# Kernel tuning notes

Measured on AMD Instinct MI355X. Metric: run time of the kernel, lower is better.

The kernel has to match this reference:

```python
import jax, jax.numpy as jnp
import numpy as np

B, DIM, W0, H0 = 4, 256, 128, 128
HEADS, HEAD_DIM = 8, 32
FOLD, PROP = 2, 4
EPS_GN = 1e-5


def _l2norm(x):
    n = jnp.linalg.norm(x, axis=-1, keepdims=True)
    return x / jnp.maximum(n, 1e-12)  # matches F.normalize eps


def _fold(t, f):
    # (b, c, f*w, f*h) -> (b*f*f, c, w, h), matching einops '(b f1 f2)' ordering
    b, c, W, H = t.shape
    w, h = W // f, H // f
    return t.reshape(b, c, f, w, f, h).transpose(0, 2, 4, 1, 3, 5).reshape(b * f * f, c, w, h)


def _unfold(t, f, b0):
    bf, c, w, h = t.shape
    return t.reshape(b0, f, f, c, w, h).transpose(0, 3, 1, 4, 2, 5).reshape(b0, c, f * w, f * h)


def _pool(t, p):
    # AdaptiveAvgPool2d((p, p)) for divisible sizes
    b, c, w, h = t.shape
    return t.reshape(b, c, p, w // p, p, h // p).mean(axis=(3, 5))


def setup_inputs() -> dict:
    key = jax.random.key(0)
    ks = jax.random.split(key, 6)
    D = HEADS * HEAD_DIM
    return {
        "x": jax.random.normal(ks[0], (B, DIM, W0, H0), jnp.float32),
        "xyz": jax.random.normal(ks[1], (B, 3, W0, H0), jnp.float32),
        "Wv": jax.random.normal(ks[2], (D, DIM, 7, 7), jnp.float32) * 0.02,
        "bv": jnp.zeros((D,), jnp.float32),
        "Wproj": jax.random.normal(ks[3], (DIM, D), jnp.float32) * 0.02,
        "bproj": jnp.zeros((DIM,), jnp.float32),
        "gn_w": jnp.ones((D,), jnp.float32),
        "gn_b": jnp.zeros((D,), jnp.float32),
        "sim_alpha": jnp.ones((1,), jnp.float32),
        "sim_beta": jnp.zeros((1,), jnp.float32),
    }


def reference(x, xyz, Wv, bv, Wproj, bproj, gn_w, gn_b, sim_alpha, sim_beta):
    # value = self.v(x): 7x7 conv, padding 3
    value = jax.lax.conv_general_dilated(
        x, Wv, (1, 1), ((3, 3), (3, 3)),
        dimension_numbers=("NCHW", "OIHW", "NCHW")) + bv[None, :, None, None]
    b0 = x.shape[0]
    # heads split: 'b (e c) w h -> (b e) c w h'
    xh = x.reshape(b0 * HEADS, HEAD_DIM, W0, H0)
    vh = value.reshape(b0 * HEADS, HEAD_DIM, W0, H0)
    xf = _fold(xh, FOLD)
    vf = _fold(vh, FOLD)
    xyzf = _fold(xyz, FOLD)
    bb, c, w, h = xf.shape
    M = PROP * PROP
    N = w * h
    centers = _pool(xf, PROP)                                   # (bb, c, p, p)
    xyz_c = _pool(xyzf, PROP)
    value_centers = _pool(vf, PROP).reshape(bb, c, M).transpose(0, 2, 1)  # (bb, M, c)
    cen = centers.reshape(bb, c, M).transpose(0, 2, 1)          # (bb, M, c)
    xpts = xf.reshape(bb, c, N).transpose(0, 2, 1)              # (bb, N, c)
    vpts = vf.reshape(bb, c, N).transpose(0, 2, 1)              # (bb, N, c)
    sim = jax.nn.sigmoid(sim_beta + sim_alpha *
                         jnp.einsum('bmc,bnc->bmn', _l2norm(cen), _l2norm(xpts)))
    bg = xyzf.shape[0]
    xyz_pts = xyzf.reshape(bg, 3, N).transpose(0, 2, 1)
    xyz_cc = xyz_c.reshape(bg, 3, M).transpose(0, 2, 1)
    sim_geo = jax.nn.sigmoid(sim_beta + sim_alpha *
                             jnp.einsum('bmc,bnc->bmn', _l2norm(xyz_cc), _l2norm(xyz_pts)))
    sim_geo = jnp.tile(sim_geo, (sim.shape[0] // sim_geo.shape[0], 1, 1))  # torch .repeat
    sim = sim * sim_geo ** 2
    # faithful mask math: scatter_(1, argmax, 1.0) into an all-ones tensor leaves it all-ones,
    # so dense_mask == 1 and split_mask == 0 exactly as in the source.
    dense_mask = jnp.ones_like(sim)
    split_mask = 1.0 - dense_mask
    denss_sim = sim * dense_mask
    split_sim = sim * split_mask
    split_out = (jnp.einsum('bmn,bnc->bmc', split_sim, vpts) + value_centers) \
                / (split_sim.sum(-1, keepdims=True) + 1.0)
    denss_out = (jnp.einsum('bmn,bnc->bmc', denss_sim, xpts) + cen) \
                / (denss_sim.sum(-1, keepdims=True) + 1.0)
    denss_pts = jnp.einsum('bmc,bmn->bnc', denss_out, denss_sim)  # (bb, N, c)
    split_pts = jnp.einsum('bmc,bmn->bnc', split_out, split_sim)
    out = (denss_pts + split_pts).transpose(0, 2, 1).reshape(bb, c, w, h)
    out = _unfold(out, FOLD, b0 * HEADS)
    out = out.reshape(b0, HEADS * HEAD_DIM, W0, H0)
    # GroupNorm with 1 group: normalize over (C, H, W) per sample
    mu = out.mean(axis=(1, 2, 3), keepdims=True)
    var = ((out - mu) ** 2).mean(axis=(1, 2, 3), keepdims=True)
    out = (out - mu) / jnp.sqrt(var + EPS_GN)
    out = out * gn_w[None, :, None, None] + gn_b[None, :, None, None]
    # proj 1x1 conv + silu
    out = jnp.einsum('bchw,oc->bohw', out, Wproj) + bproj[None, :, None, None]
    return jax.nn.silu(out)
```

## Files before the change

kernel.cpp:

```cpp
#include <hip/hip_runtime.h>
#include <stdint.h>


typedef __attribute__((ext_vector_type(8))) short short8;
typedef __attribute__((ext_vector_type(4))) float floatx4;
typedef __fp16 fp16x2 __attribute__((ext_vector_type(2)));

#define SIMW 264

__device__ float g_sbp[256];
__device__ float g_bias[1024];
__device__ __attribute__((aligned(16))) _Float16 g_Wa[4*256*256];
__device__ float g_cenraw[128*16*32];
__device__ float g_cenhat[128*16*32];
__device__ float g_gcenhat[16*16*4];
__device__ __attribute__((aligned(16))) _Float16 g_sim[(size_t)128*4096*16];
__device__ float g_dnum[128*16*16*32];
__device__ float g_Gp[(size_t)128*16*256];
__device__ float g_rsum[128*16*16];
__device__ __attribute__((aligned(16))) unsigned g_dnh2[128*256];

static __device__ __forceinline__ fp16x2 as_h2(unsigned u) { return __builtin_bit_cast(fp16x2, u); }
static __device__ __forceinline__ unsigned pk(float a, float b) {
  return __builtin_bit_cast(unsigned, __builtin_amdgcn_cvt_pkrtz(a, b));
}
static __device__ __forceinline__ float h16(float v) {
  return (float)as_h2(pk(v, 0.f))[0];
}
#if __has_builtin(__builtin_amdgcn_fdot2)
static __device__ __forceinline__ float fdot2(fp16x2 a, fp16x2 b, float c) {
  return __builtin_amdgcn_fdot2(a, b, c, false);
}
#else
static __device__ __forceinline__ float fdot2(fp16x2 a, fp16x2 b, float c) {
  return c + (float)a[0]*(float)b[0] + (float)a[1]*(float)b[1];
}
#endif
static __device__ __forceinline__ float sum16(const float* p) {
  const float4* q = (const float4*)p;
  float4 a = q[0], b = q[1], c = q[2], d = q[3];
  return (a.x+a.y+a.z+a.w) + (b.x+b.y+b.z+b.w) + (c.x+c.y+c.z+c.w) + (d.x+d.y+d.z+d.w);
}
static __device__ __forceinline__ float sigm(float z) {
  return __builtin_amdgcn_rcpf(1.f + __expf(-z));
}

__global__ __launch_bounds__(64) void k0_geo(const float* __restrict__ xyz) {
  __shared__ float gc[64];
  const int gti = blockIdx.x;
  const int bg = gti >> 2, f1 = (gti >> 1) & 1, f2 = gti & 1;
  const int t = threadIdx.x;
  if (t < 48) {
    const int m = t / 3, ch = t - 3*(t/3);
    const int pi = m >> 2, pj = m & 3;
    const float* p = xyz + (size_t)(bg*3+ch)*16384 + (f1*64 + pi*16)*128 + f2*64 + pj*16;
    float s = 0.f;
    #pragma unroll
    for (int r = 0; r < 16; ++r) s += sum16(p + r*128);
    gc[m*4+ch] = s * (1.f/256.f);
  }
  __syncthreads();
  if (t < 16) {
    float g0 = gc[t*4], g1 = gc[t*4+1], g2 = gc[t*4+2];
    float inv = 1.f / fmaxf(sqrtf(g0*g0+g1*g1+g2*g2), 1e-12f);
    float* o = g_gcenhat + gti*64 + t*4;
    o[0] = g0*inv; o[1] = g1*inv; o[2] = g2*inv; o[3] = 0.f;
  }
}

__global__ __launch_bounds__(128) void k1a_cen(const float* __restrict__ x) {
  __shared__ float cenL[128];
  __shared__ float invL[4];
  const int blk = blockIdx.x;
  const int bb = blk >> 2, pi = blk & 3;
  const int b = bb >> 5, e = (bb >> 2) & 7, f1 = (bb >> 1) & 1, f2 = bb & 1;
  const int tid = threadIdx.x;
  const int c = tid >> 2, pj = tid & 3;
  const int m = pi*4 + pj;
  const float* p = x + ((size_t)(b*256 + e*32 + c)*128 + f1*64 + pi*16)*128 + f2*64 + pj*16;
  float s = 0.f;
  #pragma unroll
  for (int r = 0; r < 16; ++r) s += sum16(p + r*128);
  const float raw = s * (1.f/256.f);
  cenL[pj*32 + c] = raw;
  g_cenraw[(bb*16 + m)*32 + c] = raw;
  __syncthreads();
  if (tid < 4) {
    float ss = 0.f;
    #pragma unroll
    for (int cc = 0; cc < 32; ++cc) { float v = cenL[tid*32+cc]; ss += v*v; }
    invL[tid] = 1.f / fmaxf(sqrtf(ss), 1e-12f);
  }
  __syncthreads();
  g_cenhat[(bb*16 + m)*32 + c] = raw * invL[pj];
}

__global__ __launch_bounds__(256, 4) void k1b_sim(const float* __restrict__ x,
                                                  const float* __restrict__ xyz,
                                                  const float* __restrict__ salpha,
                                                  const float* __restrict__ sbeta) {
  __shared__ __attribute__((aligned(16))) unsigned  xL[256*20];
  __shared__ __attribute__((aligned(16))) _Float16 simS[16*SIMW];
  __shared__ __attribute__((aligned(16))) _Float16 gT[16*SIMW];
  __shared__ __attribute__((aligned(16))) unsigned chP[16*16];
  __shared__ float gcenL[64];
  __shared__ float rsW[4*16];
  __shared__ float dnumL[512];
  float* GL = (float*)gT;
  const int blk = blockIdx.x;
  const int bb = blk >> 4, ck = blk & 15;
  const int b = bb >> 5, e = (bb >> 2) & 7, f1 = (bb >> 1) & 1, f2 = bb & 1;
  const int gti = ((e & 3) << 2) | (f1 << 1) | f2;
  const int tid = threadIdx.x, lane = tid & 63, wave = tid >> 6;
  const int lm = lane & 15, quad = lane >> 4;
  const float alpha = salpha[0], beta = sbeta[0];
  const float* xt = x + (((size_t)(b*256 + e*32))*128 + f1*64)*128 + f2*64;

  {
    const float2 cp = *(const float2*)(g_cenhat + bb*512 + tid*2);
    chP[tid] = pk(cp.x, cp.y);
  }
  if (tid < 64) gcenL[tid] = g_gcenhat[gti*64 + tid];
  dnumL[tid] = 0.f; dnumL[tid + 256] = 0.f;
  __syncthreads();

  const int ng = ck*256 + tid;
  const int wi = ng >> 6, hi = ng & 63;
  const int addr = wi*128 + hi;
  {
    float ss = 0.f;
    unsigned xp[16];
    #pragma unroll
    for (int p = 0; p < 16; ++p) {
      const float v0 = xt[(size_t)(2*p)*16384 + addr];
      const float v1 = xt[(size_t)(2*p+1)*16384 + addr];
      ss += v0*v0 + v1*v1;
      xp[p] = pk(v0, v1);
    }
    uint4 u0 = {xp[0],xp[1],xp[2],xp[3]};
    uint4 u1 = {xp[4],xp[5],xp[6],xp[7]};
    uint4 u2 = {xp[8],xp[9],xp[10],xp[11]};
    uint4 u3 = {xp[12],xp[13],xp[14],xp[15]};
    *(uint4*)(xL + tid*20)      = u0;
    *(uint4*)(xL + tid*20 + 4)  = u1;
    *(uint4*)(xL + tid*20 + 8)  = u2;
    *(uint4*)(xL + tid*20 + 12) = u3;
    const float invn = __builtin_amdgcn_rcpf(fmaxf(sqrtf(ss), 1e-12f));
    ((float*)xL)[tid*20 + 16] = invn;
  }
  {
    const float* gp = xyz + (size_t)((e & 3)*3)*16384 + (f1*64 + wi)*128 + f2*64 + hi;
    float g0 = gp[0], g1 = gp[16384], g2 = gp[32768];
    const float invg = __builtin_amdgcn_rcpf(fmaxf(sqrtf(g0*g0+g1*g1+g2*g2), 1e-12f));
    g0 *= invg; g1 *= invg; g2 *= invg;
    #pragma unroll
    for (int m = 0; m < 16; ++m) {
      const float* gh = gcenL + m*4;
      const float dg = gh[0]*g0 + gh[1]*g1 + gh[2]*g2;
      const float gg = sigm(beta + alpha*dg);
      gT[m*SIMW + tid] = (_Float16)(gg*gg);
    }
  }
  __syncthreads();

  {
    const short8 afx = *(const short8*)((const _Float16*)chP + lm*32 + quad*8);
    float rsacc[4] = {0.f, 0.f, 0.f, 0.f};
    #pragma unroll
    for (int t = 0; t < 4; ++t) {
      const int px = wave*64 + t*16 + lm;
      const short8 bfx = *(const short8*)((const _Float16*)xL + px*40 + quad*8);
      floatx4 d = {0.f,0.f,0.f,0.f};
      d = __builtin_amdgcn_mfma_f32_16x16x32_f16(afx, bfx, d, 0, 0, 0);
      const float invn = ((const float*)xL)[px*20 + 16];
      #pragma unroll
      for (int r = 0; r < 4; ++r) {
        const int m = quad*4 + r;
        const float gg2 = (float)gT[m*SIMW + px];
        const float sv = sigm(beta + alpha * d[r] * invn) * gg2;
        rsacc[r] += sv;
        simS[m*SIMW + px] = (_Float16)sv;
      }
    }
    #pragma unroll
    for (int r = 0; r < 4; ++r) {
      float v = rsacc[r];
      v += __shfl_xor(v, 1, 64); v += __shfl_xor(v, 2, 64);
      v += __shfl_xor(v, 4, 64); v += __shfl_xor(v, 8, 64);
      if (lm == 0) rsW[wave*16 + quad*4 + r] = v;
    }
  }
  __syncthreads();
  if (tid < 256) GL[tid] = 0.f;
  __syncthreads();

  {
    unsigned w[8];
    const unsigned short* sp = (const unsigned short*)simS;
    #pragma unroll
    for (int p = 0; p < 8; ++p)
      w[p] = (unsigned)sp[(2*p)*SIMW + tid] | ((unsigned)sp[(2*p+1)*SIMW + tid] << 16);
    _Float16* gp = g_sim + ((size_t)bb*4096 + ng)*16;
    *(uint4*)gp       = *(const uint4*)&w[0];
    *(uint4*)(gp + 8) = *(const uint4*)&w[4];
  }
  if (tid < 16)
    g_rsum[(bb*16 + ck)*16 + tid] = rsW[tid] + rsW[16+tid] + rsW[32+tid] + rsW[48+tid];

  {
    floatx4 acc0 = {0.f,0.f,0.f,0.f}, acc1 = {0.f,0.f,0.f,0.f};
    floatx4 accG = {0.f,0.f,0.f,0.f};
    #pragma unroll
    for (int ks = 0; ks < 2; ++ks) {
      const int kb = wave*64 + ks*32 + quad*8;
      const short8 af = *(const short8*)(simS + lm*SIMW + kb);
      const int ag = ck*512 + ((kb >> 6)*128) + (kb & 63);
      const float* pb0 = xt + (size_t)lm*16384 + ag;
      const float* pb1 = pb0 + (size_t)16*16384;
      short8 bf0, bf1;
      #pragma unroll
      for (int t = 0; t < 8; ++t) bf0[t] = __builtin_bit_cast(short, (_Float16)pb0[t]);
      #pragma unroll
      for (int t = 0; t < 8; ++t) bf1[t] = __builtin_bit_cast(short, (_Float16)pb1[t]);
      acc0 = __builtin_amdgcn_mfma_f32_16x16x32_f16(af, bf0, acc0, 0, 0, 0);
      acc1 = __builtin_amdgcn_mfma_f32_16x16x32_f16(af, bf1, acc1, 0, 0, 0);
      accG = __builtin_amdgcn_mfma_f32_16x16x32_f16(af, af,  accG, 0, 0, 0);
    }
    #pragma unroll
    for (int r = 0; r < 4; ++r) {
      atomicAdd(&dnumL[(quad*4 + r)*32 + lm],      acc0[r]);
      atomicAdd(&dnumL[(quad*4 + r)*32 + 16 + lm], acc1[r]);
      atomicAdd(&GL[(quad*4 + r)*16 + lm],         accG[r]);
    }
  }
  __syncthreads();
  g_dnum[(size_t)(bb*16 + ck)*512 + tid]       = dnumL[tid];
  g_dnum[(size_t)(bb*16 + ck)*512 + 256 + tid] = dnumL[tid + 256];
  g_Gp[(size_t)(bb*16 + ck)*256 + tid]         = GL[tid];
}

__global__ __launch_bounds__(512) void k1c_red() {
  __shared__ float denssL[512];
  __shared__ float rsL[16];
  __shared__ float red[16];
  const int bb = blockIdx.x, tid = threadIdx.x, lane = tid & 63, wv = tid >> 6;
  if (tid < 16) {
    float r = 1.f;
    #pragma unroll
    for (int k = 0; k < 16; ++k) r += g_rsum[(bb*16 + k)*16 + tid];
    rsL[tid] = r;
  }
  float a = g_cenraw[bb*512 + tid];
  #pragma unroll
  for (int k = 0; k < 16; ++k) a += g_dnum[(size_t)bb*8192 + k*512 + tid];
  __syncthreads();
  denssL[tid] = a / rsL[tid >> 5];
  __syncthreads();
  if (tid < 256) {
    const int c = tid >> 3, mp = tid & 7;
    g_dnh2[bb*256 + c*8 + mp] = pk(denssL[(2*mp)*32 + c], denssL[(2*mp+1)*32 + c]);
  }
  float contrib = 0.f;
  if (tid < 256) {
    const int m = tid >> 4, m2 = tid & 15;
    float g = 0.f;
    #pragma unroll
    for (int k = 0; k < 16; ++k) g += g_Gp[((size_t)bb*16 + k)*256 + tid];
    float p = 0.f;
    #pragma unroll
    for (int c = 0; c < 32; ++c)
      p += h16(denssL[m*32 + c]) * h16(denssL[m2*32 + c]);
    contrib = g * p;
  }
  float s1t = 0.f;
  if (tid < 16) {
    float sc = 0.f;
    #pragma unroll
    for (int c = 0; c < 32; ++c) sc += h16(denssL[tid*32 + c]);
    s1t = (rsL[tid] - 1.f) * sc;
  }
  #pragma unroll
  for (int off = 1; off < 64; off <<= 1) {
    contrib += __shfl_xor(contrib, off, 64);
    s1t     += __shfl_xor(s1t, off, 64);
  }
  if (lane == 0) { red[wv] = contrib; red[8 + wv] = s1t; }
  __syncthreads();
  if (tid == 0) {
    float s2 = 0.f, s1 = 0.f;
    #pragma unroll
    for (int w = 0; w < 8; ++w) { s2 += red[w]; s1 += red[8 + w]; }
    g_sbp[bb*2]     = s1;
    g_sbp[bb*2 + 1] = s2;
  }
}

__global__ __launch_bounds__(256) void k2_prep(const float* __restrict__ Wp,
                                               const float* __restrict__ bpr,
                                               const float* __restrict__ gnw,
                                               const float* __restrict__ gnb) {
  __shared__ float betaL[256];
  __shared__ float alphaL[256];
  __shared__ float S12[2];
  const int b = blockIdx.x, t = threadIdx.x;
  if (t < 64) {
    float v1 = 0.f, v2 = 0.f;
    if (t < 32) { v1 = g_sbp[(b*32 + t)*2]; v2 = g_sbp[(b*32 + t)*2 + 1]; }
    #pragma unroll
    for (int off = 1; off < 64; off <<= 1) { v1 += __shfl_xor(v1, off, 64); v2 += __shfl_xor(v2, off, 64); }
    if (t == 0) { S12[0] = v1; S12[1] = v2; }
  }
  __syncthreads();
  const float S1 = S12[0];
  const float S2 = S12[1];
  const float inv_n = 1.f / 4194304.f;
  const float mu  = S1 * inv_n;
  const float inv = rsqrtf(fmaxf(S2*inv_n - mu*mu, 0.f) + 1e-5f);
  const float a = inv * gnw[t];
  alphaL[t] = a;
  betaL[t] = gnb[t] - mu * a;
  __syncthreads();
  float k = bpr[t];
  const float* wr = Wp + t*256;
  _Float16* wa = g_Wa + ((size_t)b*256 + t)*256;
  for (int c = 0; c < 256; c += 8) {
    const float4 w0 = *(const float4*)(wr + c);
    const float4 w1 = *(const float4*)(wr + c + 4);
    k += w0.x*betaL[c+0] + w0.y*betaL[c+1] + w0.z*betaL[c+2] + w0.w*betaL[c+3]
       + w1.x*betaL[c+4] + w1.y*betaL[c+5] + w1.z*betaL[c+6] + w1.w*betaL[c+7];
    uint4 o;
    o.x = pk(w0.x*alphaL[c+0], w0.y*alphaL[c+1]);
    o.y = pk(w0.z*alphaL[c+2], w0.w*alphaL[c+3]);
    o.z = pk(w1.x*alphaL[c+4], w1.y*alphaL[c+5]);
    o.w = pk(w1.z*alphaL[c+6], w1.w*alphaL[c+7]);
    *(uint4*)(wa + c) = o;
  }
  g_bias[b*256 + t] = k;
}

__global__ __launch_bounds__(256, 4) void kf_proj(float* __restrict__ out) {
  __shared__ __attribute__((aligned(16))) _Float16 preL[64*256];
  __shared__ float biasL[256];
  const int blk = blockIdx.x;
  const int b = blk >> 8, pb = blk & 255;
  const int f1 = pb >> 7, f2 = pb & 1;
  const int nbase = ((pb >> 1) & 63) * 64;
  const int tid = threadIdx.x, lane = tid & 63, wave = tid >> 6;
  const int lm = lane & 15, quad = lane >> 4;
  const int m0 = wave*64;
  biasL[tid] = g_bias[b*256 + tid];

  #pragma unroll
  for (int eh = 0; eh < 2; ++eh) {
    const int e = wave*2 + eh;
    const int bb = b*32 + e*4 + f1*2 + f2;
    short8 bf0 = {}, bf1 = {};
    if (quad < 2) {
      const _Float16* dp = (const _Float16*)g_dnh2 + (size_t)bb*512 + quad*8;
      bf0 = *(const short8*)(dp + lm*16);
      bf1 = *(const short8*)(dp + (16 + lm)*16);
    }
    #pragma unroll
    for (int pt = 0; pt < 4; ++pt) {
      const short8 af = *(const short8*)(g_sim
          + ((size_t)bb*4096 + nbase + pt*16 + lm)*16 + (quad & 1)*8);
      floatx4 c0 = {0.f,0.f,0.f,0.f}, c1 = {0.f,0.f,0.f,0.f};
      c0 = __builtin_amdgcn_mfma_f32_16x16x32_f16(af, bf0, c0, 0, 0, 0);
      c1 = __builtin_amdgcn_mfma_f32_16x16x32_f16(af, bf1, c1, 0, 0, 0);
      #pragma unroll
      for (int r = 0; r < 4; ++r) {
        const int px = pt*16 + quad*4 + r;
        const int swz = (px & 7) << 4;
        const int b0 = (px*512 + (e*32 + lm)*2) ^ swz;
        const int b1 = (px*512 + (e*32 + 16 + lm)*2) ^ swz;
        *(_Float16*)((char*)preL + b0) = (_Float16)c0[r];
        *(_Float16*)((char*)preL + b1) = (_Float16)c1[r];
      }
    }
  }
  __syncthreads();

  floatx4 acc[4][4] = {};
  #pragma unroll
  for (int ks = 0; ks < 8; ++ks) {
    const _Float16* abase = g_Wa + ((size_t)b*256)*256 + (size_t)ks*32 + quad*8;
    short8 afr[4], bfr[4];
    #pragma unroll
    for (int mi = 0; mi < 4; ++mi)
      afr[mi] = *(const short8*)(abase + (size_t)(m0 + mi*16 + lm)*256);
    #pragma unroll
    for (int ni = 0; ni < 4; ++ni) {
      const int row = ni*16 + lm;
      const int byte = (row*512 + ks*64 + quad*16) ^ ((row & 7) << 4);
      bfr[ni] = *(const short8*)((const char*)preL + byte);
    }
    #pragma unroll
    for (int mi = 0; mi < 4; ++mi) {
      #pragma unroll
      for (int ni = 0; ni < 4; ++ni)
        acc[mi][ni] = __builtin_amdgcn_mfma_f32_16x16x32_f16(afr[mi], bfr[ni], acc[mi][ni], 0, 0, 0);
    }
  }
  #pragma unroll
  for (int mi = 0; mi < 4; ++mi) {
    #pragma unroll
    for (int r = 0; r < 4; ++r) {
      const int o = m0 + mi*16 + quad*4 + r;
      const float kb = biasL[o];
      #pragma unroll
      for (int ni = 0; ni < 4; ++ni) {
        float val = acc[mi][ni][r] + kb;
        val = val * sigm(val);
        out[((size_t)(b*256 + o))*16384 + pb*64 + ni*16 + lm] = val;
      }
    }
  }
}

extern "C" void kernel_launch(void* const* d_in, const int* in_sizes, int n_in,
                              void* d_out, int out_size, void* d_ws, size_t ws_size,
                              hipStream_t stream)
{
  (void)in_sizes; (void)n_in; (void)d_ws; (void)ws_size; (void)out_size;
  const float* x     = (const float*)d_in[0];
  const float* xyz   = (const float*)d_in[1];
  const float* Wproj = (const float*)d_in[4];
  const float* bproj = (const float*)d_in[5];
  const float* gnw   = (const float*)d_in[6];
  const float* gnb   = (const float*)d_in[7];
  const float* sa    = (const float*)d_in[8];
  const float* sb    = (const float*)d_in[9];
  float* out = (float*)d_out;

  hipLaunchKernelGGL(k0_geo,  dim3(16),   dim3(64),  0, stream, xyz);
  hipLaunchKernelGGL(k1a_cen, dim3(512),  dim3(128), 0, stream, x);
  hipLaunchKernelGGL(k1b_sim, dim3(2048), dim3(256), 0, stream, x, xyz, sa, sb);
  hipLaunchKernelGGL(k1c_red, dim3(128),  dim3(512), 0, stream);
  hipLaunchKernelGGL(k2_prep, dim3(4),    dim3(256), 0, stream, Wproj, bproj, gnw, gnb);
  hipLaunchKernelGGL(kf_proj, dim3(1024), dim3(256), 0, stream, out);
}
```

Before: 260.1 us.

## Merge pooling kernels, drop gT buffer and LDS atomics in sim kernel

Merges the xyz-pooling and x-pooling kernels into one launch with block-range dispatch. In the similarity kernel, the per-pixel geometric gate is no longer precomputed into a shared fp16 table; it is recomputed inline from normalized xyz stored next to the inverse norm. The LDS atomicAdd reduction of the MFMA partials is replaced by per-wave stores into an overlay of the xL buffer followed by a plain 4-way sum. Together these cut shared-memory use enough to raise launch bounds to 5 blocks per CU. The trade-off is some redundant sigmoid work per quad and reuse of xL after a barrier.

```diff
diff --git a/kernel.cpp b/kernel.cpp
--- a/kernel.cpp
+++ b/kernel.cpp
@@ -45,68 +45,66 @@
   return __builtin_amdgcn_rcpf(1.f + __expf(-z));
 }
 
-__global__ __launch_bounds__(64) void k0_geo(const float* __restrict__ xyz) {
-  __shared__ float gc[64];
-  const int gti = blockIdx.x;
-  const int bg = gti >> 2, f1 = (gti >> 1) & 1, f2 = gti & 1;
-  const int t = threadIdx.x;
-  if (t < 48) {
-    const int m = t / 3, ch = t - 3*(t/3);
-    const int pi = m >> 2, pj = m & 3;
-    const float* p = xyz + (size_t)(bg*3+ch)*16384 + (f1*64 + pi*16)*128 + f2*64 + pj*16;
-    float s = 0.f;
-    #pragma unroll
-    for (int r = 0; r < 16; ++r) s += sum16(p + r*128);
-    gc[m*4+ch] = s * (1.f/256.f);
-  }
-  __syncthreads();
-  if (t < 16) {
-    float g0 = gc[t*4], g1 = gc[t*4+1], g2 = gc[t*4+2];
-    float inv = 1.f / fmaxf(sqrtf(g0*g0+g1*g1+g2*g2), 1e-12f);
-    float* o = g_gcenhat + gti*64 + t*4;
-    o[0] = g0*inv; o[1] = g1*inv; o[2] = g2*inv; o[3] = 0.f;
-  }
-}
-
-__global__ __launch_bounds__(128) void k1a_cen(const float* __restrict__ x) {
+__global__ __launch_bounds__(128) void k01_pool(const float* __restrict__ x,
+                                                const float* __restrict__ xyz) {
   __shared__ float cenL[128];
   __shared__ float invL[4];
+  __shared__ float gc[64];
   const int blk = blockIdx.x;
-  const int bb = blk >> 2, pi = blk & 3;
-  const int b = bb >> 5, e = (bb >> 2) & 7, f1 = (bb >> 1) & 1, f2 = bb & 1;
   const int tid = threadIdx.x;
-  const int c = tid >> 2, pj = tid & 3;
-  const int m = pi*4 + pj;
-  const float* p = x + ((size_t)(b*256 + e*32 + c)*128 + f1*64 + pi*16)*128 + f2*64 + pj*16;
-  float s = 0.f;
-  #pragma unroll
-  for (int r = 0; r < 16; ++r) s += sum16(p + r*128);
-  const float raw = s * (1.f/256.f);
-  cenL[pj*32 + c] = raw;
-  g_cenraw[(bb*16 + m)*32 + c] = raw;
-  __syncthreads();
-  if (tid < 4) {
-    float ss = 0.f;
-    #pragma unroll
-    for (int cc = 0; cc < 32; ++cc) { float v = cenL[tid*32+cc]; ss += v*v; }
-    invL[tid] = 1.f / fmaxf(sqrtf(ss), 1e-12f);
-  }
-  __syncthreads();
-  g_cenhat[(bb*16 + m)*32 + c] = raw * invL[pj];
-}
-
-__global__ __launch_bounds__(256, 4) void k1b_sim(const float* __restrict__ x,
+  if (blk < 512) {
+    const int bb = blk >> 2, pi = blk & 3;
+    const int b = bb >> 5, e = (bb >> 2) & 7, f1 = (bb >> 1) & 1, f2 = bb & 1;
+    const int c = tid >> 2, pj = tid & 3;
+    const int m = pi*4 + pj;
+    const float* p = x + ((size_t)(b*256 + e*32 + c)*128 + f1*64 + pi*16)*128 + f2*64 + pj*16;
+    float s = 0.f;
+    #pragma unroll
+    for (int r = 0; r < 16; ++r) s += sum16(p + r*128);
+    const float raw = s * (1.f/256.f);
+    cenL[pj*32 + c] = raw;
+    g_cenraw[(bb*16 + m)*32 + c] = raw;
+    __syncthreads();
+    if (tid < 4) {
+      float ss = 0.f;
+      #pragma unroll
+      for (int cc = 0; cc < 32; ++cc) { float v = cenL[tid*32+cc]; ss += v*v; }
+      invL[tid] = 1.f / fmaxf(sqrtf(ss), 1e-12f);
+    }
+    __syncthreads();
+    g_cenhat[(bb*16 + m)*32 + c] = raw * invL[pj];
+  } else {
+    const int gti = blk - 512;
+    const int bg = gti >> 2, f1 = (gti >> 1) & 1, f2 = gti & 1;
+    if (tid < 48) {
+      const int m = tid / 3, ch = tid - 3*(tid/3);
+      const int pi = m >> 2, pj = m & 3;
+      const float* p = xyz + (size_t)(bg*3+ch)*16384 + (f1*64 + pi*16)*128 + f2*64 + pj*16;
+      float s = 0.f;
+      #pragma unroll
+      for (int r = 0; r < 16; ++r) s += sum16(p + r*128);
+      gc[m*4+ch] = s * (1.f/256.f);
+    }
+    __syncthreads();
+    if (tid < 16) {
+      float g0 = gc[tid*4], g1 = gc[tid*4+1], g2 = gc[tid*4+2];
+      float inv = 1.f / fmaxf(sqrtf(g0*g0+g1*g1+g2*g2), 1e-12f);
+      float* o = g_gcenhat + gti*64 + tid*4;
+      o[0] = g0*inv; o[1] = g1*inv; o[2] = g2*inv; o[3] = 0.f;
+    }
+  }
+}
+
+__global__ __launch_bounds__(256, 5) void k1b_sim(const float* __restrict__ x,
                                                   const float* __restrict__ xyz,
                                                   const float* __restrict__ salpha,
                                                   const float* __restrict__ sbeta) {
   __shared__ __attribute__((aligned(16))) unsigned  xL[256*20];
   __shared__ __attribute__((aligned(16))) _Float16 simS[16*SIMW];
-  __shared__ __attribute__((aligned(16))) _Float16 gT[16*SIMW];
   __shared__ __attribute__((aligned(16))) unsigned chP[16*16];
   __shared__ float gcenL[64];
-  __shared__ float rsW[4*16];
-  __shared__ float dnumL[512];
-  float* GL = (float*)gT;
+  __shared__ float rsW[64];
+  float* ovl = (float*)xL;
   const int blk = blockIdx.x;
   const int bb = blk >> 4, ck = blk & 15;
   const int b = bb >> 5, e = (bb >> 2) & 7, f1 = (bb >> 1) & 1, f2 = bb & 1;
@@ -121,7 +119,6 @@
     chP[tid] = pk(cp.x, cp.y);
   }
   if (tid < 64) gcenL[tid] = g_gcenhat[gti*64 + tid];
-  dnumL[tid] = 0.f; dnumL[tid + 256] = 0.f;
   __syncthreads();
 
   const int ng = ck*256 + tid;
@@ -146,20 +143,11 @@
     *(uint4*)(xL + tid*20 + 8)  = u2;
     *(uint4*)(xL + tid*20 + 12) = u3;
     const float invn = __builtin_amdgcn_rcpf(fmaxf(sqrtf(ss), 1e-12f));
-    ((float*)xL)[tid*20 + 16] = invn;
-  }
-  {
     const float* gp = xyz + (size_t)((e & 3)*3)*16384 + (f1*64 + wi)*128 + f2*64 + hi;
     float g0 = gp[0], g1 = gp[16384], g2 = gp[32768];
     const float invg = __builtin_amdgcn_rcpf(fmaxf(sqrtf(g0*g0+g1*g1+g2*g2), 1e-12f));
-    g0 *= invg; g1 *= invg; g2 *= invg;
-    #pragma unroll
-    for (int m = 0; m < 16; ++m) {
-      const float* gh = gcenL + m*4;
-      const float dg = gh[0]*g0 + gh[1]*g1 + gh[2]*g2;
-      const float gg = sigm(beta + alpha*dg);
-      gT[m*SIMW + tid] = (_Float16)(gg*gg);
-    }
+    float4 tail = {invn, g0*invg, g1*invg, g2*invg};
+    *(float4*)((float*)xL + tid*20 + 16) = tail;
   }
   __syncthreads();
 
@@ -172,12 +160,14 @@
       const short8 bfx = *(const short8*)((const _Float16*)xL + px*40 + quad*8);
       floatx4 d = {0.f,0.f,0.f,0.f};
       d = __builtin_amdgcn_mfma_f32_16x16x32_f16(afx, bfx, d, 0, 0, 0);
-      const float invn = ((const float*)xL)[px*20 + 16];
+      const float4 ig = *(const float4*)((const float*)xL + px*20 + 16);
       #pragma unroll
       for (int r = 0; r < 4; ++r) {
         const int m = quad*4 + r;
-        const float gg2 = (float)gT[m*SIMW + px];
-        const float sv = sigm(beta + alpha * d[r] * invn) * gg2;
+        const float* gh = gcenL + m*4;
+        const float dg = gh[0]*ig.y + gh[1]*ig.z + gh[2]*ig.w;
+        const float gg = sigm(beta + alpha*dg);
+        const float sv = sigm(beta + alpha * d[r] * ig.x) * gg * gg;
         rsacc[r] += sv;
         simS[m*SIMW + px] = (_Float16)sv;
       }
@@ -190,8 +180,6 @@
       if (lm == 0) rsW[wave*16 + quad*4 + r] = v;
     }
   }
-  __syncthreads();
-  if (tid < 256) GL[tid] = 0.f;
   __syncthreads();
 
   {
@@ -228,15 +216,22 @@
     }
     #pragma unroll
     for (int r = 0; r < 4; ++r) {
-      atomicAdd(&dnumL[(quad*4 + r)*32 + lm],      acc0[r]);
-      atomicAdd(&dnumL[(quad*4 + r)*32 + 16 + lm], acc1[r]);
-      atomicAdd(&GL[(quad*4 + r)*16 + lm],         accG[r]);
-    }
-  }
-  __syncthreads();
-  g_dnum[(size_t)(bb*16 + ck)*512 + tid]       = dnumL[tid];
-  g_dnum[(size_t)(bb*16 + ck)*512 + 256 + tid] = dnumL[tid + 256];
-  g_Gp[(size_t)(bb*16 + ck)*256 + tid]         = GL[tid];
+      const int m = quad*4 + r;
+      ovl[wave*512 + m*32 + lm]        = acc0[r];
+      ovl[wave*512 + m*32 + 16 + lm]   = acc1[r];
+      ovl[2048 + wave*256 + m*16 + lm] = accG[r];
+    }
+  }
+  __syncthreads();
+
+  {
+    const float d0 = ovl[tid]       + ovl[512 + tid]  + ovl[1024 + tid] + ovl[1536 + tid];
+    const float d1 = ovl[256 + tid] + ovl[768 + tid]  + ovl[1280 + tid] + ovl[1792 + tid];
+    g_dnum[(size_t)(bb*16 + ck)*512 + tid]       = d0;
+    g_dnum[(size_t)(bb*16 + ck)*512 + 256 + tid] = d1;
+    const float gsum = ovl[2048 + tid] + ovl[2304 + tid] + ovl[2560 + tid] + ovl[2816 + tid];
+    g_Gp[(size_t)(bb*16 + ck)*256 + tid] = gsum;
+  }
 }
 
 __global__ __launch_bounds__(512) void k1c_red() {
@@ -432,10 +427,9 @@
   const float* sb    = (const float*)d_in[9];
   float* out = (float*)d_out;
 
-  hipLaunchKernelGGL(k0_geo,  dim3(16),   dim3(64),  0, stream, xyz);
-  hipLaunchKernelGGL(k1a_cen, dim3(512),  dim3(128), 0, stream, x);
-  hipLaunchKernelGGL(k1b_sim, dim3(2048), dim3(256), 0, stream, x, xyz, sa, sb);
-  hipLaunchKernelGGL(k1c_red, dim3(128),  dim3(512), 0, stream);
-  hipLaunchKernelGGL(k2_prep, dim3(4),    dim3(256), 0, stream, Wproj, bproj, gnw, gnb);
-  hipLaunchKernelGGL(kf_proj, dim3(1024), dim3(256), 0, stream, out);
-}
+  hipLaunchKernelGGL(k01_pool, dim3(528),  dim3(128), 0, stream, x, xyz);
+  hipLaunchKernelGGL(k1b_sim,  dim3(2048), dim3(256), 0, stream, x, xyz, sa, sb);
+  hipLaunchKernelGGL(k1c_red,  dim3(128),  dim3(512), 0, stream);
+  hipLaunchKernelGGL(k2_prep,  dim3(4),    dim3(256), 0, stream, Wproj, bproj, gnw, gnb);
+  hipLaunchKernelGGL(kf_proj,  dim3(1024), dim3(256), 0, stream, out);
+}
```

After: 235.2 us. -9.6%, faster.
